# Performance work log

Hardware: AMD Instinct MI355X
Metric: run time of the kernel (lower is better)

## Reference

```python
import jax, jax.numpy as jnp
import numpy as np

EPS = 1e-6
H = 16  # heads

def rmsnorm(x, w):
    return x * jax.lax.rsqrt(jnp.mean(x * x, axis=-1, keepdims=True) + EPS) * w

def l2norm(x):
    return x * jax.lax.rsqrt(jnp.sum(x * x, axis=-1, keepdims=True) + EPS)

def setup_inputs() -> dict:
    key = jax.random.key(0)
    ks = jax.random.split(key, 12)
    B, S, D, F = 2, 2048, 1024, 4096
    std = 0.02
    inp = {
        'hidden_states': jax.random.normal(ks[0], (B, S, D), jnp.float32),
        'Wq': jax.random.normal(ks[1], (D, D), jnp.float32) * std,
        'Wk': jax.random.normal(ks[2], (D, D), jnp.float32) * std,
        'Wv': jax.random.normal(ks[3], (D, D), jnp.float32) * std,
        'Wb': jax.random.normal(ks[4], (D, H), jnp.float32) * std,
        'Wo': jax.random.normal(ks[5], (D, D), jnp.float32) * std,
        'ln1': jnp.ones((D,), jnp.float32),
        'ln2': jnp.ones((D,), jnp.float32),
        'Wg': jax.random.normal(ks[6], (D, F), jnp.float32) * std,
        'Wu': jax.random.normal(ks[7], (D, F), jnp.float32) * std,
        'Wd': jax.random.normal(ks[8], (F, D), jnp.float32) * std,
    }
    return inp

def delta_rule(q, k, v, beta):
    # q,k: [B,S,H,dk] (l2-normalized), v: [B,S,H,dv], beta: [B,S,H]
    B, S, Hh, dk = q.shape
    dv = v.shape[-1]
    # time-major for scan: [S,B,H,...]
    qt = jnp.moveaxis(q, 1, 0)
    kt = jnp.moveaxis(k, 1, 0)
    vt = jnp.moveaxis(v, 1, 0)
    bt = jnp.moveaxis(beta, 1, 0)

    def step(Sm, inp):
        qi, ki, vi, bi = inp  # [B,H,dk],[B,H,dk],[B,H,dv],[B,H]
        Sk = jnp.einsum('bhkv,bhk->bhv', Sm, ki)          # S^T k
        upd = ki[..., :, None] * (vi - Sk)[..., None, :]  # outer(k, v - S^T k)
        Sm = Sm + bi[..., None, None] * upd
        oi = jnp.einsum('bhkv,bhk->bhv', Sm, qi)
        return Sm, oi

    S0 = jnp.zeros((B, Hh, dk, dv), q.dtype)
    _, out = jax.lax.scan(step, S0, (qt, kt, vt, bt))
    return jnp.moveaxis(out, 0, 1)  # [B,S,H,dv]

def reference(hidden_states, Wq, Wk, Wv, Wb, Wo, ln1, ln2, Wg, Wu, Wd):
    B, S, D = hidden_states.shape
    dk = D // H
    # --- delta-rule attention sub-block ---
    x = rmsnorm(hidden_states, ln1)
    q = l2norm(jax.nn.silu(x @ Wq).reshape(B, S, H, dk))
    k = l2norm(jax.nn.silu(x @ Wk).reshape(B, S, H, dk))
    v = jax.nn.silu(x @ Wv).reshape(B, S, H, dk)
    beta = jax.nn.sigmoid(x @ Wb)  # [B,S,H]
    o = delta_rule(q, k, v, beta).reshape(B, S, D)
    h = hidden_states + o @ Wo
    # --- SwiGLU MLP sub-block ---
    y = rmsnorm(h, ln2)
    h = h + (jax.nn.silu(y @ Wg) * (y @ Wu)) @ Wd
    return h
```

## Files before the change

kernel.cpp:

```cpp
#include <hip/hip_runtime.h>
#include <hip/hip_bf16.h>
#include <stdint.h>

#define BB 2
#define SS 2048
#define DD 1024
#define FF 4096
#define HH 16
#define ROWS (BB*SS)
#define NC 32
#define NQKV 3200

typedef float f32x4 __attribute__((ext_vector_type(4)));
typedef __bf16 bf16x8 __attribute__((ext_vector_type(8)));

typedef __attribute__((address_space(1))) const void* gas1p;
typedef __attribute__((address_space(3))) void* las3p;

__device__ __forceinline__ void gload16(const void* g, void* l) {
    __builtin_amdgcn_global_load_lds((gas1p)g, (las3p)l, 16, 0, 0);
}

__device__ __forceinline__ unsigned short f2bf(float f) {
    unsigned int u = __builtin_bit_cast(unsigned int, f);
    u += 0x7fffu + ((u >> 16) & 1u);
    return (unsigned short)(u >> 16);
}
__device__ __forceinline__ float bf2f(unsigned short s) {
    unsigned int u = ((unsigned int)s) << 16;
    return __builtin_bit_cast(float, u);
}
__device__ __forceinline__ float sigmoidf_(float x) { return 1.f / (1.f + __expf(-x)); }
__device__ __forceinline__ float siluf_(float x)    { return x / (1.f + __expf(-x)); }

__device__ __forceinline__ int swz(int b) { return b ^ (((b >> 7) & 7) << 4); }

__device__ __forceinline__ void tp_body(const float* __restrict__ W,
                                        unsigned short* __restrict__ Wt,
                                        int K, int N, int bx, int by, int tid) {
    __shared__ float tile[32][33];
    int tx = tid & 31, ty = tid >> 5;
    int n0 = bx * 32, k0 = by * 32;
#pragma unroll
    for (int i = 0; i < 4; ++i)
        tile[ty + 8 * i][tx] = W[(size_t)(k0 + ty + 8 * i) * N + n0 + tx];
    __syncthreads();
#pragma unroll
    for (int i = 0; i < 4; ++i)
        Wt[(size_t)(n0 + ty + 8 * i) * K + k0 + tx] = f2bf(tile[tx][ty + 8 * i]);
}

__global__ __launch_bounds__(256) void transpose_cvt(const float* __restrict__ W,
                                                     unsigned short* __restrict__ Wt,
                                                     int K, int N) {
    tp_body(W, Wt, K, N, blockIdx.x, blockIdx.y, threadIdx.x);
}

__global__ __launch_bounds__(256) void transpose_cvt4(const float* W0, const float* W1,
                                                      const float* W2, const float* W3,
                                                      unsigned short* T0, unsigned short* T1,
                                                      unsigned short* T2, unsigned short* T3) {
    const float* W = (blockIdx.z == 0) ? W0 : (blockIdx.z == 1) ? W1 : (blockIdx.z == 2) ? W2 : W3;
    unsigned short* T = (blockIdx.z == 0) ? T0 : (blockIdx.z == 1) ? T1 : (blockIdx.z == 2) ? T2 : T3;
    tp_body(W, T, DD, DD, blockIdx.x, blockIdx.y, threadIdx.x);
}

__global__ __launch_bounds__(256) void transpose_cvt_gu(const float* W0, const float* W1,
                                                        unsigned short* Wt) {
    const float* W = (blockIdx.z == 0) ? W0 : W1;
    int isU = blockIdx.z;
    __shared__ float tile[32][33];
    int tid = threadIdx.x;
    int tx = tid & 31, ty = tid >> 5;
    int n0 = blockIdx.x * 32, k0 = blockIdx.y * 32;
#pragma unroll
    for (int i = 0; i < 4; ++i)
        tile[ty + 8 * i][tx] = W[(size_t)(k0 + ty + 8 * i) * FF + n0 + tx];
    __syncthreads();
#pragma unroll
    for (int i = 0; i < 4; ++i) {
        int j = n0 + ty + 8 * i;
        int rint = ((j >> 4) << 5) + (j & 15) + (isU << 4);
        Wt[(size_t)rint * DD + k0 + tx] = f2bf(tile[tx][ty + 8 * i]);
    }
}

__global__ __launch_bounds__(256) void wbt_kernel(const float* __restrict__ Wb,
                                                  unsigned short* __restrict__ WbT) {
    int idx = blockIdx.x * 256 + threadIdx.x;
    int d = idx >> 4, h = idx & 15;
    WbT[h * DD + d] = f2bf(Wb[idx]);
}

__global__ __launch_bounds__(256) void rmsnorm_bf16_kernel(const float* __restrict__ src,
                                                           const float* __restrict__ w,
                                                           unsigned short* __restrict__ dst) {
    int row = blockIdx.x;
    int tid = threadIdx.x;
    float4 x = ((const float4*)(src + (size_t)row * DD))[tid];
    float ss = x.x * x.x + x.y * x.y + x.z * x.z + x.w * x.w;
#pragma unroll
    for (int m = 1; m < 64; m <<= 1) ss += __shfl_xor(ss, m, 64);
    __shared__ float ws4[4];
    if ((tid & 63) == 0) ws4[tid >> 6] = ss;
    __syncthreads();
    ss = ws4[0] + ws4[1] + ws4[2] + ws4[3];
    float sc = rsqrtf(ss * (1.f / DD) + 1e-6f);
    float4 wv = ((const float4*)w)[tid];
    ushort4 o;
    o.x = f2bf(x.x * sc * wv.x);
    o.y = f2bf(x.y * sc * wv.y);
    o.z = f2bf(x.z * sc * wv.z);
    o.w = f2bf(x.w * sc * wv.w);
    ((ushort4*)(dst + (size_t)row * DD))[tid] = o;
}

template <int EP, int BMt, int BNt, int WM, int WN, bool FASTM>
__global__ __launch_bounds__(WM * WN * 64) void gemm2(const unsigned short* __restrict__ A,
                                                      const unsigned short* __restrict__ Bt,
                                                      const float* __restrict__ res,
                                                      float* __restrict__ cf,
                                                      unsigned short* __restrict__ cb,
                                                      int M, int N, int K) {
    constexpr int NW = WM * WN;
    constexpr int MI = BMt / (WM * 16);
    constexpr int NI = BNt / (WN * 16);
    constexpr int ACH = BMt / 8 / NW;
    constexpr int BCH = BNt / 8 / NW;
    constexpr int ABYTES = BMt * 128;
    constexpr int BBYTES = BNt * 128;
    __shared__ __align__(16) char lds[2 * (ABYTES + BBYTES)];

    int tid = threadIdx.x, lane = tid & 63, w = tid >> 6;
    int wm = w / WN, wn = w % WN;

    int gm = M / BMt, gn = N / BNt, nwg = gm * gn;
    int flat = blockIdx.x;
    int q = nwg >> 3, r8 = nwg & 7;
    int xcd = flat & 7, loc = flat >> 3;
    int sid = (xcd < r8 ? xcd * (q + 1) : r8 * (q + 1) + (xcd - r8) * q) + loc;
    int midx, nidx;
    if (FASTM) { midx = sid % gm; nidx = sid / gm; }
    else       { nidx = sid % gn; midx = sid / gn; }
    int m0 = midx * BMt, n0 = nidx * BNt;

    auto stage = [&](int buf, int kt) {
        char* base = (char*)lds + buf * (ABYTES + BBYTES);
        int row8 = lane >> 3, col = (lane & 7) * 8;
#pragma unroll
        for (int i = 0; i < ACH; ++i) {
            int c = w * ACH + i;
            gload16(A + ((size_t)(m0 + c * 8 + row8) * K + kt * 64 + col), base + c * 1024);
        }
#pragma unroll
        for (int i = 0; i < BCH; ++i) {
            int c = w * BCH + i;
            gload16(Bt + ((size_t)(n0 + c * 8 + row8) * K + kt * 64 + col), base + ABYTES + c * 1024);
        }
    };

    f32x4 acc[MI][NI] = {};
    int nk = K / 64;
    stage(0, 0);
    __syncthreads();
    int cur = 0;
    for (int kt = 0; kt < nk; ++kt) {
        if (kt + 1 < nk) stage(cur ^ 1, kt + 1);
        const char* abuf = (const char*)lds + cur * (ABYTES + BBYTES);
        const char* bbuf = abuf + ABYTES;
#pragma unroll
        for (int kk = 0; kk < 2; ++kk) {
            bf16x8 afr[MI], bfr[NI];
#pragma unroll
            for (int mi = 0; mi < MI; ++mi)
                afr[mi] = *(const bf16x8*)(abuf + (wm * (MI * 16) + mi * 16 + (lane & 15)) * 128 + kk * 64 + (lane >> 4) * 16);
#pragma unroll
            for (int ni = 0; ni < NI; ++ni)
                bfr[ni] = *(const bf16x8*)(bbuf + (wn * (NI * 16) + ni * 16 + (lane & 15)) * 128 + kk * 64 + (lane >> 4) * 16);
#pragma unroll
            for (int mi = 0; mi < MI; ++mi)
#pragma unroll
                for (int ni = 0; ni < NI; ++ni)
                    acc[mi][ni] = __builtin_amdgcn_mfma_f32_16x16x32_bf16(afr[mi], bfr[ni], acc[mi][ni], 0, 0, 0);
        }
        if (kt + 1 < nk) {
            __syncthreads();
            cur ^= 1;
        }
    }

    int mbase = m0 + wm * (MI * 16) + (lane >> 4) * 4;
    if (EP == 4) {
        int j0 = (n0 + wn * (NI * 16)) / 2 + (lane & 15);
#pragma unroll
        for (int mi = 0; mi < MI; ++mi)
#pragma unroll
            for (int p = 0; p < NI / 2; ++p)
#pragma unroll
                for (int r = 0; r < 4; ++r) {
                    int m = mbase + mi * 16 + r;
                    float gv = acc[mi][2 * p][r], uv = acc[mi][2 * p + 1][r];
                    cb[(size_t)m * FF + j0 + 16 * p] = f2bf(siluf_(gv) * uv);
                }
    } else {
        int nbase = n0 + wn * (NI * 16) + (lane & 15);
#pragma unroll
        for (int mi = 0; mi < MI; ++mi)
#pragma unroll
            for (int ni = 0; ni < NI; ++ni)
#pragma unroll
                for (int r = 0; r < 4; ++r) {
                    int m = mbase + mi * 16 + r;
                    int n = nbase + ni * 16;
                    float v = acc[mi][ni][r];
                    if (EP == 3) {
                        int seg = n >> 10, col = n & 1023;
                        if (seg < 3)
                            cb[(size_t)seg * ROWS * DD + (size_t)m * DD + col] = f2bf(v);
                        else if (col < 16)
                            cf[(size_t)m * HH + col] = sigmoidf_(v);
                    } else {
                        if (EP == 1) v += res[(size_t)m * N + n];
                        if (EP == 2) cb[(size_t)m * N + n] = f2bf(v);
                        else         cf[(size_t)m * N + n] = v;
                    }
                }
    }
}


__device__ __forceinline__ bf16x8 ldsfrag(const char* mat, int row, int kt, int lane) {
    return *(const bf16x8*)(mat + swz(row * 128 + kt * 64 + (lane >> 4) * 16));
}

template <bool INIT_P>
__device__ __forceinline__ void mm64(const char* X, const char* Y, const char* P,
                                     f32x4 acc[4], int w, int lane) {
    int g = lane >> 4;
#pragma unroll
    for (int j = 0; j < 4; ++j) {
        if (INIT_P) {
#pragma unroll
            for (int r = 0; r < 4; ++r) {
                int m = 16 * w + g * 4 + r, n = (lane & 15) + 16 * j;
                acc[j][r] = bf2f(*(const unsigned short*)(P + swz(m * 128 + n * 2)));
            }
        } else {
            acc[j] = (f32x4){0.f, 0.f, 0.f, 0.f};
        }
    }
    bf16x8 xs0 = ldsfrag(X, 16 * w + (lane & 15), 0, lane);
    bf16x8 xs1 = ldsfrag(X, 16 * w + (lane & 15), 1, lane);
#pragma unroll
    for (int j = 0; j < 4; ++j) {
        bf16x8 y0 = ldsfrag(Y, 16 * j + (lane & 15), 0, lane);
        bf16x8 y1 = ldsfrag(Y, 16 * j + (lane & 15), 1, lane);
        acc[j] = __builtin_amdgcn_mfma_f32_16x16x32_bf16(xs0, y0, acc[j], 0, 0, 0);
        acc[j] = __builtin_amdgcn_mfma_f32_16x16x32_bf16(xs1, y1, acc[j], 0, 0, 0);
    }
}

__device__ __forceinline__ void wR(char* D, const f32x4 acc[4], int w, int lane, int mode) {
    int g = lane >> 4;
#pragma unroll
    for (int j = 0; j < 4; ++j)
#pragma unroll
        for (int r = 0; r < 4; ++r) {
            int m = 16 * w + g * 4 + r, n = (lane & 15) + 16 * j;
            float v = acc[j][r];
            if (mode >= 1) v = (n < m) ? v : 0.f;
            if (mode == 2) v = ((m == n) ? 1.f : 0.f) - v;
            *(unsigned short*)(D + swz(m * 128 + n * 2)) = f2bf(v);
        }
}

__device__ __forceinline__ void wT(char* D, const f32x4 acc[4], int w, int lane, int mode) {
    int g = lane >> 4;
#pragma unroll
    for (int j = 0; j < 4; ++j) {
        int n = (lane & 15) + 16 * j, m0 = 16 * w + g * 4;
        ushort4 pk;
        pk.x = (mode == 1 && !(n < m0 + 0)) ? (unsigned short)0 : f2bf(acc[j][0]);
        pk.y = (mode == 1 && !(n < m0 + 1)) ? (unsigned short)0 : f2bf(acc[j][1]);
        pk.z = (mode == 1 && !(n < m0 + 2)) ? (unsigned short)0 : f2bf(acc[j][2]);
        pk.w = (mode == 1 && !(n < m0 + 3)) ? (unsigned short)0 : f2bf(acc[j][3]);
        *(ushort4*)(D + swz(n * 128 + m0 * 2)) = pk;
    }
}

__device__ __forceinline__ void load16bf(const unsigned short* p, float* v) {
    uint4 a = *(const uint4*)p, b = *(const uint4*)(p + 8);
    unsigned int u0[8] = {a.x, a.y, a.z, a.w, b.x, b.y, b.z, b.w};
#pragma unroll
    for (int i = 0; i < 8; ++i) {
        v[2 * i]     = bf2f((unsigned short)(u0[i] & 0xffffu));
        v[2 * i + 1] = bf2f((unsigned short)(u0[i] >> 16));
    }
}

__global__ __launch_bounds__(256) void delta_prep_kernel(const unsigned short* __restrict__ qb,
                                                         const unsigned short* __restrict__ kb,
                                                         const unsigned short* __restrict__ vb,
                                                         const float* __restrict__ betab,
                                                         char* __restrict__ chunkbuf) {
    __shared__ __align__(16) char sK[8192], sKb[8192], sKbT[8192], sVbT[8192], sQ[8192];
    __shared__ __align__(16) char mA[8192], mAT[8192], mB2[8192], mBT[8192], mP0[8192], mP1[8192];

    int ci = blockIdx.x;
    int c = ci & 31, h = (ci >> 5) & 15, b = ci >> 9;
    int tid = threadIdx.x;
    int lane = tid & 63, w = tid >> 6;

    char* cbuf = chunkbuf + (size_t)ci * 40960;
    unsigned short* Qg  = (unsigned short*)(cbuf);
    unsigned short* KTg = (unsigned short*)(cbuf + 8192);
    unsigned short* Ag  = (unsigned short*)(cbuf + 16384);
    unsigned short* Wg  = (unsigned short*)(cbuf + 24576);
    unsigned short* U0g = (unsigned short*)(cbuf + 32768);

    {
        int trow = tid >> 2, part = tid & 3, d0 = part * 16;
        size_t rg = (size_t)b * SS + c * 64 + trow;
        float bet = betab[rg * HH + h];
        size_t base = rg * DD + h * 64 + d0;

        float qv[16], kv[16], vv[16];
        load16bf(qb + base, qv);
        load16bf(kb + base, kv);
        load16bf(vb + base, vv);

        float ssq = 0.f, ssk = 0.f;
#pragma unroll
        for (int i = 0; i < 16; ++i) {
            qv[i] = siluf_(qv[i]); ssq += qv[i] * qv[i];
            kv[i] = siluf_(kv[i]); ssk += kv[i] * kv[i];
            vv[i] = siluf_(vv[i]);
        }
        ssq += __shfl_xor(ssq, 1, 64); ssq += __shfl_xor(ssq, 2, 64);
        ssk += __shfl_xor(ssk, 1, 64); ssk += __shfl_xor(ssk, 2, 64);
        float scq = rsqrtf(ssq + 1e-6f), sck = rsqrtf(ssk + 1e-6f);
#pragma unroll
        for (int i = 0; i < 16; ++i) { qv[i] *= scq; kv[i] *= sck; }

#pragma unroll
        for (int m = 0; m < 4; ++m) {
            ushort4 pq, pk_, pkb;
#pragma unroll
            for (int r = 0; r < 4; ++r) {
                ((unsigned short*)&pq)[r]  = f2bf(qv[4 * m + r]);
                ((unsigned short*)&pk_)[r] = f2bf(kv[4 * m + r]);
                ((unsigned short*)&pkb)[r] = f2bf(bet * kv[4 * m + r]);
            }
            int bo = trow * 128 + (d0 + 4 * m) * 2;
            *(ushort4*)(sQ + swz(bo))  = pq;
            *(ushort4*)(sK + swz(bo))  = pk_;
            *(ushort4*)(sKb + swz(bo)) = pkb;
            *(ushort4*)(Qg + trow * 64 + d0 + 4 * m) = pq;
        }
#pragma unroll
        for (int e = 0; e < 16; ++e) {
            int d = d0 + e;
            *(unsigned short*)(sKbT + swz(d * 128 + trow * 2)) = f2bf(bet * kv[e]);
            *(unsigned short*)(sVbT + swz(d * 128 + trow * 2)) = f2bf(bet * vv[e]);
            KTg[d * 64 + trow] = f2bf(kv[e]);
        }
    }
    __syncthreads();

    f32x4 acc[4];
    mm64<false>(sKb, sK, nullptr, acc, w, lane);
    wR(mA, acc, w, lane, 1);
    wT(mAT, acc, w, lane, 1);
    wR(mP0, acc, w, lane, 2);
    __syncthreads();

    char *cX = mA, *cXT = mAT, *nX = mB2, *nXT = mBT, *pc = mP0, *pn = mP1;
#pragma unroll
    for (int s = 0; s < 5; ++s) {
        mm64<false>(cX, cXT, nullptr, acc, w, lane);
        wR(nX, acc, w, lane, 0);
        wT(nXT, acc, w, lane, 0);
        __syncthreads();
        mm64<true>(pc, nXT, pc, acc, w, lane);
        wR(pn, acc, w, lane, 0);
        __syncthreads();
        char* t;
        t = cX; cX = nX; nX = t;
        t = cXT; cXT = nXT; nXT = t;
        t = pc; pc = pn; pn = t;
    }

    int g = lane >> 4;
    mm64<false>(sK, sQ, nullptr, acc, w, lane);
#pragma unroll
    for (int j = 0; j < 4; ++j) {
        int n = (lane & 15) + 16 * j, m0 = 16 * w + g * 4;
        ushort4 pk;
        pk.x = (m0 + 0 <= n) ? f2bf(acc[j][0]) : (unsigned short)0;
        pk.y = (m0 + 1 <= n) ? f2bf(acc[j][1]) : (unsigned short)0;
        pk.z = (m0 + 2 <= n) ? f2bf(acc[j][2]) : (unsigned short)0;
        pk.w = (m0 + 3 <= n) ? f2bf(acc[j][3]) : (unsigned short)0;
        *(ushort4*)(Ag + n * 64 + m0) = pk;
    }
    mm64<false>(sKbT, pc, nullptr, acc, w, lane);
#pragma unroll
    for (int j = 0; j < 4; ++j) {
        int n = (lane & 15) + 16 * j, m0 = 16 * w + g * 4;
        ushort4 pk;
        pk.x = f2bf(acc[j][0]); pk.y = f2bf(acc[j][1]);
        pk.z = f2bf(acc[j][2]); pk.w = f2bf(acc[j][3]);
        *(ushort4*)(Wg + n * 64 + m0) = pk;
    }
    mm64<false>(pc, sVbT, nullptr, acc, w, lane);
#pragma unroll
    for (int j = 0; j < 4; ++j) {
        int n = (lane & 15) + 16 * j, m0 = 16 * w + g * 4;
        ushort4 pk;
        pk.x = f2bf(acc[j][0]); pk.y = f2bf(acc[j][1]);
        pk.z = f2bf(acc[j][2]); pk.w = f2bf(acc[j][3]);
        *(ushort4*)(U0g + n * 64 + m0) = pk;
    }
}

__global__ __launch_bounds__(256) void delta_seq_kernel(const char* __restrict__ chunkbuf,
                                                        unsigned short* __restrict__ ob) {
    __shared__ __align__(16) char stg[2 * 40960 + 8192 + 8192];
    int bh = blockIdx.x;
    int b = bh >> 4, h = bh & 15;
    int tid = threadIdx.x;
    int lane = tid & 63, w = tid >> 6, g = lane >> 4;

    char* UTw = stg + 81920 + w * 2048;
    char* Slw = stg + 90112 + w * 2048;

    f32x4 s_acc[4];
#pragma unroll
    for (int j = 0; j < 4; ++j) s_acc[j] = (f32x4){0.f, 0.f, 0.f, 0.f};
    uint4 z4 = {0, 0, 0, 0};
    *(uint4*)(Slw + lane * 32) = z4;
    *(uint4*)(Slw + lane * 32 + 16) = z4;

    const char* cbase = chunkbuf + (size_t)bh * NC * 40960;
    int lo = (lane * 16) ^ ((lane >> 3) << 4);
    int pw = 10 * w;

    {
        const char* src = cbase;
        char* dst = stg;
#pragma unroll
        for (int p = 0; p < 10; ++p)
            gload16(src + (pw + p) * 1024 + lo, dst + (pw + p) * 1024);
    }

    for (int c = 0; c < NC; ++c) {
        {
            const char* src = cbase + (size_t)((c + 1) & 31) * 40960;
            char* dst = stg + ((c + 1) & 1) * 40960;
#pragma unroll
            for (int p = 0; p < 10; ++p)
                gload16(src + (pw + p) * 1024 + lo, dst + (pw + p) * 1024);
        }
        asm volatile("s_waitcnt vmcnt(10)" ::: "memory");
        __builtin_amdgcn_s_barrier();
        __builtin_amdgcn_sched_barrier(0);

        const char* cur = stg + (c & 1) * 40960;
        const char* Qm = cur, *KTm = cur + 8192, *Am = cur + 16384, *Wm = cur + 24576, *U0m = cur + 32768;

        bf16x8 xs0 = ldsfrag(Slw, lane & 15, 0, lane);
        bf16x8 xs1 = ldsfrag(Slw, lane & 15, 1, lane);

        f32x4 ut[4];
        f32x4 oa[4];
#pragma unroll
        for (int j = 0; j < 4; ++j) { ut[j] = (f32x4){0.f, 0.f, 0.f, 0.f}; oa[j] = (f32x4){0.f, 0.f, 0.f, 0.f}; }
#pragma unroll
        for (int j = 0; j < 4; ++j) {
            bf16x8 y0 = ldsfrag(Wm, 16 * j + (lane & 15), 0, lane);
            bf16x8 y1 = ldsfrag(Wm, 16 * j + (lane & 15), 1, lane);
            ut[j] = __builtin_amdgcn_mfma_f32_16x16x32_bf16(xs0, y0, ut[j], 0, 0, 0);
            ut[j] = __builtin_amdgcn_mfma_f32_16x16x32_bf16(xs1, y1, ut[j], 0, 0, 0);
        }
#pragma unroll
        for (int j = 0; j < 4; ++j) {
            bf16x8 y0 = ldsfrag(Qm, 16 * j + (lane & 15), 0, lane);
            bf16x8 y1 = ldsfrag(Qm, 16 * j + (lane & 15), 1, lane);
            oa[j] = __builtin_amdgcn_mfma_f32_16x16x32_bf16(xs0, y0, oa[j], 0, 0, 0);
            oa[j] = __builtin_amdgcn_mfma_f32_16x16x32_bf16(xs1, y1, oa[j], 0, 0, 0);
        }
#pragma unroll
        for (int j = 0; j < 4; ++j)
#pragma unroll
            for (int r = 0; r < 4; ++r) {
                int m = 16 * w + g * 4 + r;
                int n = (lane & 15) + 16 * j;
                float u0 = bf2f(*(const unsigned short*)(U0m + swz(m * 128 + n * 2)));
                float u = u0 - ut[j][r];
                *(unsigned short*)(UTw + swz((g * 4 + r) * 128 + n * 2)) = f2bf(u);
            }
        bf16x8 us0 = ldsfrag(UTw, lane & 15, 0, lane);
        bf16x8 us1 = ldsfrag(UTw, lane & 15, 1, lane);
#pragma unroll
        for (int j = 0; j < 4; ++j) {
            bf16x8 y0 = ldsfrag(Am, 16 * j + (lane & 15), 0, lane);
            bf16x8 y1 = ldsfrag(Am, 16 * j + (lane & 15), 1, lane);
            oa[j] = __builtin_amdgcn_mfma_f32_16x16x32_bf16(us0, y0, oa[j], 0, 0, 0);
            oa[j] = __builtin_amdgcn_mfma_f32_16x16x32_bf16(us1, y1, oa[j], 0, 0, 0);
        }
#pragma unroll
        for (int j = 0; j < 4; ++j) {
            bf16x8 y0 = ldsfrag(KTm, 16 * j + (lane & 15), 0, lane);
            bf16x8 y1 = ldsfrag(KTm, 16 * j + (lane & 15), 1, lane);
            s_acc[j] = __builtin_amdgcn_mfma_f32_16x16x32_bf16(us0, y0, s_acc[j], 0, 0, 0);
            s_acc[j] = __builtin_amdgcn_mfma_f32_16x16x32_bf16(us1, y1, s_acc[j], 0, 0, 0);
        }
#pragma unroll
        for (int j = 0; j < 4; ++j) {
            int n = (lane & 15) + 16 * j;
            size_t tg = (size_t)b * SS + c * 64 + n;
            int col = h * 64 + 16 * w + g * 4;
            ushort4 pk;
            pk.x = f2bf(oa[j][0]); pk.y = f2bf(oa[j][1]);
            pk.z = f2bf(oa[j][2]); pk.w = f2bf(oa[j][3]);
            *(ushort4*)(ob + tg * DD + col) = pk;
        }
#pragma unroll
        for (int j = 0; j < 4; ++j)
#pragma unroll
            for (int r = 0; r < 4; ++r) {
                int n = (lane & 15) + 16 * j;
                *(unsigned short*)(Slw + swz((g * 4 + r) * 128 + n * 2)) = f2bf(s_acc[j][r]);
            }

        asm volatile("" ::: "memory");
        __builtin_amdgcn_s_barrier();
        __builtin_amdgcn_sched_barrier(0);
    }
}

extern "C" void kernel_launch(void* const* d_in, const int* in_sizes, int n_in,
                              void* d_out, int out_size, void* d_ws, size_t ws_size,
                              hipStream_t stream) {
    const float* hidden = (const float*)d_in[0];
    const float* Wq  = (const float*)d_in[1];
    const float* Wk  = (const float*)d_in[2];
    const float* Wv  = (const float*)d_in[3];
    const float* Wb  = (const float*)d_in[4];
    const float* Wo  = (const float*)d_in[5];
    const float* ln1 = (const float*)d_in[6];
    const float* ln2 = (const float*)d_in[7];
    const float* Wg  = (const float*)d_in[8];
    const float* Wu  = (const float*)d_in[9];
    const float* Wd  = (const float*)d_in[10];
    float* out = (float*)d_out;
    char* ws = (char*)d_ws;

    const size_t MB = 1024 * 1024;
    const size_t KB256 = 262144;
    unsigned short* wq_t = (unsigned short*)(ws + 0 * MB);
    unsigned short* wk_t = (unsigned short*)(ws + 2 * MB);
    unsigned short* wv_t = (unsigned short*)(ws + 4 * MB);
    unsigned short* wbT  = (unsigned short*)(ws + 6 * MB);
    unsigned short* wo_t = (unsigned short*)(ws + 6 * MB + KB256);
    unsigned short* btGU = (unsigned short*)(ws + 8 * MB + KB256);
    unsigned short* wd_t = (unsigned short*)(ws + 24 * MB + KB256);
    float* hbuf          = (float*)(ws + 32 * MB + KB256);
    unsigned short* yb   = (unsigned short*)(ws + 48 * MB + KB256);
    unsigned short* qb   = (unsigned short*)(ws + 56 * MB + KB256);
    unsigned short* kb   = (unsigned short*)(ws + 64 * MB + KB256);
    unsigned short* vb   = (unsigned short*)(ws + 72 * MB + KB256);
    float* betab         = (float*)(ws + 80 * MB + KB256);
    unsigned short* xb   = (unsigned short*)(ws + 80 * MB + 2 * KB256);
    unsigned short* ob   = xb;
    char* chunkbuf       = ws + 88 * MB + 2 * KB256;
    unsigned short* act  = (unsigned short*)(ws + 56 * MB + KB256);

    dim3 blk(256);

    transpose_cvt4<<<dim3(32, 32, 4), blk, 0, stream>>>(Wq, Wk, Wv, Wo, wq_t, wk_t, wv_t, wo_t);
    transpose_cvt_gu<<<dim3(128, 32, 2), blk, 0, stream>>>(Wg, Wu, btGU);
    transpose_cvt<<<dim3(32, 128), blk, 0, stream>>>(Wd, wd_t, FF, DD);
    wbt_kernel<<<64, blk, 0, stream>>>(Wb, wbT);

    rmsnorm_bf16_kernel<<<ROWS, blk, 0, stream>>>(hidden, ln1, xb);

    gemm2<3, 128, 128, 2, 2, false><<<dim3((NQKV / 128) * (ROWS / 128)), blk, 0, stream>>>(
        xb, wq_t, nullptr, betab, qb, ROWS, NQKV, DD);

    delta_prep_kernel<<<1024, blk, 0, stream>>>(qb, kb, vb, betab, chunkbuf);
    delta_seq_kernel<<<BB * HH, blk, 0, stream>>>(chunkbuf, ob);

    gemm2<1, 128, 128, 2, 2, false><<<dim3((DD / 128) * (ROWS / 128)), blk, 0, stream>>>(
        ob, wo_t, hidden, hbuf, nullptr, ROWS, DD, DD);

    rmsnorm_bf16_kernel<<<ROWS, blk, 0, stream>>>(hbuf, ln2, yb);

    gemm2<4, 256, 256, 2, 4, true><<<dim3((2 * FF / 256) * (ROWS / 256)), dim3(512), 0, stream>>>(
        yb, btGU, nullptr, nullptr, act, ROWS, 2 * FF, DD);

    gemm2<1, 128, 128, 2, 2, false><<<dim3((DD / 128) * (ROWS / 128)), blk, 0, stream>>>(
        act, wd_t, hbuf, out, nullptr, ROWS, DD, FF);
}
```

Measured before the change: 464.2 us.

## Add dedicated 4-stage pipelined GEMM kernel for fused gate/up SwiGLU projection

Replaces the generic gemm2 instantiation for the gate/up projection with a specialized 256x256 kernel. It uses a 4-deep LDS ring of BK=32 stages, issues async loads three stages ahead with explicit vmcnt waits, and splits the MFMA work into two halves interleaved with the next stage's A and B loads. It also remaps workgroups across the XCDs and raises wave priority around the MFMA blocks. This is meant to hide global-to-LDS latency for the largest GEMM, at the cost of more LDS, tighter register pressure and hand-tuned barrier and waitcnt logic that could be fragile.

```diff
diff --git a/kernel.cpp b/kernel.cpp
--- a/kernel.cpp
+++ b/kernel.cpp
@@ -190,42 +190,130 @@
     }
 
     int mbase = m0 + wm * (MI * 16) + (lane >> 4) * 4;
-    if (EP == 4) {
-        int j0 = (n0 + wn * (NI * 16)) / 2 + (lane & 15);
-#pragma unroll
-        for (int mi = 0; mi < MI; ++mi)
-#pragma unroll
-            for (int p = 0; p < NI / 2; ++p)
-#pragma unroll
-                for (int r = 0; r < 4; ++r) {
-                    int m = mbase + mi * 16 + r;
-                    float gv = acc[mi][2 * p][r], uv = acc[mi][2 * p + 1][r];
-                    cb[(size_t)m * FF + j0 + 16 * p] = f2bf(siluf_(gv) * uv);
+    int nbase = n0 + wn * (NI * 16) + (lane & 15);
+#pragma unroll
+    for (int mi = 0; mi < MI; ++mi)
+#pragma unroll
+        for (int ni = 0; ni < NI; ++ni)
+#pragma unroll
+            for (int r = 0; r < 4; ++r) {
+                int m = mbase + mi * 16 + r;
+                int n = nbase + ni * 16;
+                float v = acc[mi][ni][r];
+                if (EP == 3) {
+                    int seg = n >> 10, col = n & 1023;
+                    if (seg < 3)
+                        cb[(size_t)seg * ROWS * DD + (size_t)m * DD + col] = f2bf(v);
+                    else if (col < 16)
+                        cf[(size_t)m * HH + col] = sigmoidf_(v);
+                } else {
+                    if (EP == 1) v += res[(size_t)m * N + n];
+                    if (EP == 2) cb[(size_t)m * N + n] = f2bf(v);
+                    else         cf[(size_t)m * N + n] = v;
                 }
-    } else {
-        int nbase = n0 + wn * (NI * 16) + (lane & 15);
-#pragma unroll
-        for (int mi = 0; mi < MI; ++mi)
-#pragma unroll
-            for (int ni = 0; ni < NI; ++ni)
-#pragma unroll
-                for (int r = 0; r < 4; ++r) {
-                    int m = mbase + mi * 16 + r;
-                    int n = nbase + ni * 16;
-                    float v = acc[mi][ni][r];
-                    if (EP == 3) {
-                        int seg = n >> 10, col = n & 1023;
-                        if (seg < 3)
-                            cb[(size_t)seg * ROWS * DD + (size_t)m * DD + col] = f2bf(v);
-                        else if (col < 16)
-                            cf[(size_t)m * HH + col] = sigmoidf_(v);
-                    } else {
-                        if (EP == 1) v += res[(size_t)m * N + n];
-                        if (EP == 2) cb[(size_t)m * N + n] = f2bf(v);
-                        else         cf[(size_t)m * N + n] = v;
-                    }
-                }
-    }
+            }
+}
+
+__global__ __launch_bounds__(512, 2) void gemm8_gu(const unsigned short* __restrict__ A,
+                                                   const unsigned short* __restrict__ Bt,
+                                                   unsigned short* __restrict__ cb,
+                                                   int M, int N, int K) {
+    __shared__ __align__(16) char lds8[4 * 32768];
+    int tid = threadIdx.x, lane = tid & 63, w = tid >> 6;
+    int wm = w >> 2, wn = w & 3;
+
+    int gm = M / 256, gn = N / 256, nwg = gm * gn;
+    int flat = blockIdx.x;
+    int q = nwg >> 3, r8 = nwg & 7;
+    int xcd = flat & 7, loc = flat >> 3;
+    int sid = (xcd < r8 ? xcd * (q + 1) : r8 * (q + 1) + (xcd - r8) * q) + loc;
+    int midx = sid % gm, nidx = sid / gm;
+    int m0 = midx * 256, n0 = nidx * 256;
+
+    int rl = tid >> 2;
+    int sc = ((tid & 3) ^ (rl & 3)) * 8;
+    auto stA = [&](int kt) {
+        char* dst = lds8 + (kt & 3) * 32768;
+        const unsigned short* src = A + (size_t)(m0 + rl) * K + kt * 32 + sc;
+        gload16(src, dst + tid * 16);
+        gload16(src + (size_t)128 * K, dst + 8192 + tid * 16);
+    };
+    auto stB = [&](int kt) {
+        char* dst = lds8 + (kt & 3) * 32768 + 16384;
+        const unsigned short* src = Bt + (size_t)(n0 + rl) * K + kt * 32 + sc;
+        gload16(src, dst + tid * 16);
+        gload16(src + (size_t)128 * K, dst + 8192 + tid * 16);
+    };
+    auto rdA = [&](const char* Ab, int mi) -> bf16x8 {
+        int b = (wm * 128 + mi * 16 + (lane & 15)) * 64 + (lane >> 4) * 16;
+        return *(const bf16x8*)(Ab + (b ^ (((b >> 6) & 3) << 4)));
+    };
+    auto rdB = [&](const char* Bb, int ni) -> bf16x8 {
+        int b = (wn * 64 + ni * 16 + (lane & 15)) * 64 + (lane >> 4) * 16;
+        return *(const bf16x8*)(Bb + (b ^ (((b >> 6) & 3) << 4)));
+    };
+
+    f32x4 acc[8][4] = {};
+    int nk = K / 32;
+
+    stA(0); stB(0); stA(1); stB(1); stA(2); stB(2);
+
+    for (int kt = 0; kt < nk; ++kt) {
+        int rem = nk - 1 - kt;
+        if (rem >= 2)      asm volatile("s_waitcnt vmcnt(8)" ::: "memory");
+        else if (rem == 1) asm volatile("s_waitcnt vmcnt(4)" ::: "memory");
+        else               asm volatile("s_waitcnt vmcnt(0)" ::: "memory");
+        __builtin_amdgcn_s_barrier();
+        __builtin_amdgcn_sched_barrier(0);
+        const char* Ab = lds8 + (kt & 3) * 32768;
+        const char* Bb = Ab + 16384;
+
+        bf16x8 bfr[4];
+        {
+            bf16x8 af[4];
+#pragma unroll
+            for (int mi = 0; mi < 4; ++mi) af[mi] = rdA(Ab, mi);
+#pragma unroll
+            for (int ni = 0; ni < 4; ++ni) bfr[ni] = rdB(Bb, ni);
+            if (kt + 3 < nk) stA(kt + 3);
+            __builtin_amdgcn_s_barrier();
+            __builtin_amdgcn_s_setprio(1);
+#pragma unroll
+            for (int mi = 0; mi < 4; ++mi)
+#pragma unroll
+                for (int ni = 0; ni < 4; ++ni)
+                    acc[mi][ni] = __builtin_amdgcn_mfma_f32_16x16x32_bf16(af[mi], bfr[ni], acc[mi][ni], 0, 0, 0);
+            __builtin_amdgcn_s_setprio(0);
+            __builtin_amdgcn_s_barrier();
+        }
+        {
+            bf16x8 af[4];
+#pragma unroll
+            for (int mi = 0; mi < 4; ++mi) af[mi] = rdA(Ab, mi + 4);
+            if (kt + 3 < nk) stB(kt + 3);
+            __builtin_amdgcn_s_barrier();
+            __builtin_amdgcn_s_setprio(1);
+#pragma unroll
+            for (int mi = 0; mi < 4; ++mi)
+#pragma unroll
+                for (int ni = 0; ni < 4; ++ni)
+                    acc[mi + 4][ni] = __builtin_amdgcn_mfma_f32_16x16x32_bf16(af[mi], bfr[ni], acc[mi + 4][ni], 0, 0, 0);
+            __builtin_amdgcn_s_setprio(0);
+        }
+    }
+
+    int j0 = (n0 + wn * 64) / 2 + (lane & 15);
+    int mb = m0 + wm * 128 + (lane >> 4) * 4;
+#pragma unroll
+    for (int mi = 0; mi < 8; ++mi)
+#pragma unroll
+        for (int p = 0; p < 2; ++p)
+#pragma unroll
+            for (int r = 0; r < 4; ++r) {
+                int m = mb + mi * 16 + r;
+                float gv = acc[mi][2 * p][r], uv = acc[mi][2 * p + 1][r];
+                cb[(size_t)m * FF + j0 + 16 * p] = f2bf(siluf_(gv) * uv);
+            }
 }
 
 
@@ -595,8 +683,8 @@
 
     rmsnorm_bf16_kernel<<<ROWS, blk, 0, stream>>>(hbuf, ln2, yb);
 
-    gemm2<4, 256, 256, 2, 4, true><<<dim3((2 * FF / 256) * (ROWS / 256)), dim3(512), 0, stream>>>(
-        yb, btGU, nullptr, nullptr, act, ROWS, 2 * FF, DD);
+    gemm8_gu<<<dim3((ROWS / 256) * (2 * FF / 256)), dim3(512), 0, stream>>>(
+        yb, btGU, act, ROWS, 2 * FF, DD);
 
     gemm2<1, 128, 128, 2, 2, false><<<dim3((DD / 128) * (ROWS / 128)), blk, 0, stream>>>(
         act, wd_t, hbuf, out, nullptr, ROWS, DD, FF);
```

After: 456.1 us. Within noise of the previous version (-1.8%).
